# Kernel tuning notes

Measured on AMD Instinct MI355X. Metric: run time of the kernel, lower is better.

## Reference

```python
import jax, jax.numpy as jnp
import numpy as np

THRESHOLD = 1.0
CURRENT_DECAY = 0.5
VOLTAGE_DECAY = 0.5
WEIGHT_SCALE = 2.0  # slayer block weight_scale=2, weight_norm=False


def spike_fn(v):
    # Heaviside spike with hard threshold (forward only)
    return (v >= THRESHOLD).astype(v.dtype)


def conv_transpose_2d(x, w):
    # x: [NT, Cin, H, W]; w: [Cin, Cout, k, k] (pytorch ConvTranspose2d layout)
    # Equivalent dilated conv: swap in/out, flip spatial taps.
    rhs = jnp.transpose(w, (1, 0, 2, 3))[:, :, ::-1, ::-1]
    return jax.lax.conv_general_dilated(
        x, rhs, window_strides=(1, 1), padding=[(1, 1), (1, 1)],
        lhs_dilation=(2, 2), dimension_numbers=('NCHW', 'OIHW', 'NCHW'))


def cuba_block(x, w):
    # x: [N, Cin, H, W, T] -> spikes [N, Cout, 2H-1, 2W-1, T]
    N, Cin, H, W, T = x.shape
    xt = jnp.transpose(x, (4, 0, 1, 2, 3)).reshape(T * N, Cin, H, W)
    z = conv_transpose_2d(xt, WEIGHT_SCALE * w)  # synapse over all timesteps at once
    Cout, Ho, Wo = z.shape[1], z.shape[2], z.shape[3]
    z = z.reshape(T, N, Cout, Ho, Wo)

    def step(carry, zt):
        cur, vol = carry
        cur = (1.0 - CURRENT_DECAY) * cur + zt          # CUBA current dynamics
        vol = (1.0 - VOLTAGE_DECAY) * vol + cur          # CUBA voltage dynamics
        s = spike_fn(vol)
        vol = vol * (1.0 - s)                            # reset voltage on spike
        return (cur, vol), s

    init = (jnp.zeros_like(z[0]), jnp.zeros_like(z[0]))
    _, spikes = jax.lax.scan(step, init, z)              # [T, N, Cout, Ho, Wo]
    return jnp.transpose(spikes, (1, 2, 3, 4, 0))


def setup_inputs() -> dict:
    key = jax.random.key(0)
    k1, k2, k3, k4 = jax.random.split(key, 4)
    c_hid, C = 32, 2
    spike = (jax.random.uniform(k1, (4, c_hid * 4, 16, 16, 32)) < 0.3).astype(jnp.float32)

    def winit(k, cin, cout):
        return jax.random.normal(k, (cin, cout, 3, 3), jnp.float32) / np.sqrt(cin * 9.0)

    return {
        'spike': spike,
        'w1': winit(k2, c_hid * 4, c_hid * 2),
        'w2': winit(k3, c_hid * 2, c_hid),
        'w3': winit(k4, c_hid, C),
    }


def reference(spike, w1, w2, w3):
    counts = []
    for w in (w1, w2, w3):
        spike = cuba_block(spike, w)
        counts.append(jnp.mean(spike))
    return spike, jnp.stack(counts).reshape(1, -1)
```

## Files before the change

kernel.cpp:

```cpp
#include <hip/hip_runtime.h>

#define TT 32

__device__ __forceinline__ float bf16_bits_to_f32(unsigned short u) {
    unsigned v = ((unsigned)u) << 16; float f; __builtin_memcpy(&f, &v, 4); return f;
}
__device__ __forceinline__ unsigned short f32_to_bf16_rne(float f) {
    unsigned u; __builtin_memcpy(&u, &f, 4);
    u += 0x7FFFu + ((u >> 16) & 1u);
    return (unsigned short)(u >> 16);
}
__device__ __forceinline__ float round_bf16_f32(float f) {
    return bf16_bits_to_f32(f32_to_bf16_rne(f));
}
__device__ __forceinline__ float f64_to_bf16_f32(double d) {
    float fz = __double2float_rz(d);
    if ((double)fz != d) {
        unsigned u; __builtin_memcpy(&u, &fz, 4); u |= 1u; __builtin_memcpy(&fz, &u, 4);
    }
    return round_bf16_f32(fz);
}
__device__ __forceinline__ unsigned spread4(unsigned b) {
    unsigned x = (b | (b << 12)) & 0x000F000Fu;
    x = (x | (x << 6)) & 0x03030303u;
    x = (x | (x << 3)) & 0x11111111u;
    return x;
}

__global__ void detect_and_init(const unsigned* __restrict__ spk,
                                int* __restrict__ flag, float* __restrict__ sums)
{
    unsigned w = spk[threadIdx.x];
    bool ok = (w == 0u) || (w == 0x3F800000u);
    unsigned long long vote = __ballot(ok);
    if (threadIdx.x == 0) {
        flag[0] = (vote == 0xFFFFFFFFFFFFFFFFull) ? 0 : 1;
        sums[0] = 0.f; sums[1] = 0.f; sums[2] = 0.f;
    }
}

__global__ __launch_bounds__(256)
void pack_interleave(const void* __restrict__ ginv, unsigned* __restrict__ idx0,
                     const int* __restrict__ flag)
{
    const int gid = blockIdx.x * 256 + threadIdx.x;
    if (gid >= 32768) return;
    const int site = gid & 255;
    const int g    = (gid >> 8) & 31;
    const int n    = gid >> 13;

    unsigned m[4];
    #pragma unroll
    for (int k = 0; k < 4; ++k) {
        const size_t ebase = ((size_t)(n * 128 + 4 * g + k) * 256 + site) * TT;
        unsigned mask = 0u;
        if (flag[0]) {
            const uint4* p = (const uint4*)((const unsigned short*)ginv + ebase);
            #pragma unroll
            for (int q = 0; q < 4; ++q) {
                uint4 a = p[q];
                unsigned wd[4] = {a.x, a.y, a.z, a.w};
                #pragma unroll
                for (int mm = 0; mm < 4; ++mm) {
                    const int t = q * 8 + mm * 2;
                    mask |= (wd[mm] & 0xFFFFu) ? (1u << t)       : 0u;
                    mask |= (wd[mm] >> 16)     ? (1u << (t + 1)) : 0u;
                }
            }
        } else {
            const float4* p = (const float4*)((const float*)ginv + ebase);
            #pragma unroll
            for (int j = 0; j < 8; ++j) {
                float4 v = p[j];
                mask |= (v.x != 0.f) ? (1u << (j * 4 + 0)) : 0u;
                mask |= (v.y != 0.f) ? (1u << (j * 4 + 1)) : 0u;
                mask |= (v.z != 0.f) ? (1u << (j * 4 + 2)) : 0u;
                mask |= (v.w != 0.f) ? (1u << (j * 4 + 3)) : 0u;
            }
        }
        m[k] = mask;
    }
    unsigned w[4];
    #pragma unroll
    for (int q = 0; q < 4; ++q)
        w[q] =  spread4((m[0] >> (8 * q)) & 0xFFu)
             | (spread4((m[1] >> (8 * q)) & 0xFFu) << 1)
             | (spread4((m[2] >> (8 * q)) & 0xFFu) << 2)
             | (spread4((m[3] >> (8 * q)) & 0xFFu) << 3);
    *(uint2*)(idx0 + (size_t)gid * 2)           = make_uint2(w[0], w[1]);
    *(uint2*)(idx0 + (size_t)(32768 + gid) * 2) = make_uint2(w[2], w[3]);
}

template<int C, int PLANE>
__global__ __launch_bounds__(256)
void pack_mid_pairs(const unsigned* __restrict__ masks, unsigned* __restrict__ idx)
{
    constexpr int G = C / 4;
    constexpr int TOT = 4 * G * PLANE;
    const int gid = blockIdx.x * 256 + threadIdx.x;
    if (gid >= TOT) return;
    const int site = gid % PLANE;
    const int g    = (gid / PLANE) % G;
    const int n    = gid / (PLANE * G);
    unsigned m[4];
    #pragma unroll
    for (int k = 0; k < 4; ++k)
        m[k] = masks[(n * C + 4 * g + k) * PLANE + site];
    unsigned w[4];
    #pragma unroll
    for (int q = 0; q < 4; ++q)
        w[q] =  spread4((m[0] >> (8 * q)) & 0xFFu)
             | (spread4((m[1] >> (8 * q)) & 0xFFu) << 1)
             | (spread4((m[2] >> (8 * q)) & 0xFFu) << 2)
             | (spread4((m[3] >> (8 * q)) & 0xFFu) << 3);
    *(uint2*)(idx + (size_t)gid * 2)         = make_uint2(w[0], w[1]);
    *(uint2*)(idx + (size_t)(TOT + gid) * 2) = make_uint2(w[2], w[3]);
}

template<int C, int PLANE>
__global__ __launch_bounds__(256)
void pack_mid(const unsigned* __restrict__ masks, unsigned* __restrict__ idx)
{
    constexpr int G = C / 4;
    constexpr int TOT = 4 * G * PLANE;
    const int gid = blockIdx.x * 256 + threadIdx.x;
    if (gid >= TOT) return;
    const int site = gid % PLANE;
    const int g    = (gid / PLANE) % G;
    const int n    = gid / (PLANE * G);
    unsigned m[4];
    #pragma unroll
    for (int k = 0; k < 4; ++k)
        m[k] = masks[(n * C + 4 * g + k) * PLANE + site];
    #pragma unroll
    for (int q = 0; q < 4; ++q) {
        const unsigned w =  spread4((m[0] >> (8 * q)) & 0xFFu)
                         | (spread4((m[1] >> (8 * q)) & 0xFFu) << 1)
                         | (spread4((m[2] >> (8 * q)) & 0xFFu) << 2)
                         | (spread4((m[3] >> (8 * q)) & 0xFFu) << 3);
        idx[q * TOT + gid] = w;
    }
}

template<int CIN, int COUT>
__global__ __launch_bounds__(256)
void cuba_layer2(const unsigned* __restrict__ idxIn, const void* __restrict__ wptr,
                 unsigned* __restrict__ maskOut, int N, int Hi, int Wi,
                 float* __restrict__ sumOut, const int* __restrict__ flag)
{
    constexpr int G = CIN / 4;
    const bool isbf = (flag[0] != 0);
    const int Ho = 2 * Hi - 1, Wo = 2 * Wi - 1;
    const int co = (int)blockIdx.y;
    const int zz = 3 - (int)blockIdx.z;
    const int po = zz >> 1, pw = zz & 1;
    const int lg = po + pw;
    const int nTap = 1 << lg;
    const int nH = Hi - po, nW = Wi - pw;
    const int sites = N * nH * nW;
    const int siteBase = (int)blockIdx.x * 256;
    if (siteBase >= sites) return;

    __shared__ double lut[G][4][16];
    {
        const unsigned short* w16 = (const unsigned short*)wptr;
        const float* w32 = (const float*)wptr;
        const int entries = G * nTap * 16;
        for (int e = threadIdx.x; e < entries; e += 256) {
            const int idx = e & 15;
            const int tp  = (e >> 4) & (nTap - 1);
            const int g   = e >> (4 + lg);
            const int v = (po && (tp >= (pw ? 2 : 1))) ? 1 : 0;
            const int h = pw ? (tp & 1) : 0;
            const int kh = v ? 0 : (po ? 2 : 1);
            const int kw = h ? 0 : (pw ? 2 : 1);
            const int wof = kh * 3 + kw;
            double s = 0.0;
            #pragma unroll
            for (int k = 0; k < 4; ++k) {
                if ((idx >> k) & 1) {
                    const int wi = ((4 * g + k) * COUT + co) * 9 + wof;
                    const float wraw = isbf ? bf16_bits_to_f32(w16[wi]) : w32[wi];
                    s += 2.0 * (double)wraw;
                }
            }
            lut[g][tp][idx] = s;
        }
    }
    __syncthreads();

    const int siteIdx = siteBase + (int)threadIdx.x;
    float cnt = 0.f;

    if (siteIdx < sites) {
        const int b  = siteIdx % nW;
        const int t1 = siteIdx / nW;
        const int a  = t1 % nH;
        const int n  = t1 / nH;
        const int oh = 2 * a + po, ow = 2 * b + pw;
        const int plane = Hi * Wi;
        const int QT = N * G * plane;

        const int siteA = a * Wi + b;
        const int siteB = siteA + 1;
        const int siteC = siteA + Wi;
        const int siteD = siteC + 1;

        unsigned mask = 0u;
        float  curF = 0.f, volF = 0.f;
        double curD = 0.0, volD = 0.0;

        #pragma unroll 1
        for (int p = 0; p < 2; ++p) {
            double acc[16];
            #pragma unroll
            for (int j = 0; j < 16; ++j) acc[j] = 0.0;

            const unsigned* pb = idxIn + (size_t)(p * QT + n * G * plane) * 2;
            for (int g = 0; g < G; ++g) {
                const unsigned* bp = pb + (size_t)g * plane * 2;

                auto doTap = [&](int site, int tp) {
                    const uint2 wv = *(const uint2*)(bp + (size_t)site * 2);
                    const double* lp = &lut[g][tp][0];
                    #pragma unroll
                    for (int j = 0; j < 8; ++j)
                        acc[j] += lp[(wv.x >> (4 * j)) & 0xFu];
                    #pragma unroll
                    for (int j = 0; j < 8; ++j)
                        acc[8 + j] += lp[(wv.y >> (4 * j)) & 0xFu];
                };

                doTap(siteA, 0);
                if (pw) doTap(siteB, 1);
                if (po) {
                    doTap(siteC, pw ? 2 : 1);
                    if (pw) doTap(siteD, 3);
                }
            }

            if (isbf) {
                #pragma unroll
                for (int j = 0; j < 16; ++j) {
                    const int t = p * 16 + j;
                    const float z = f64_to_bf16_f32(acc[j]);
                    curF = round_bf16_f32(0.5f * curF + z);
                    volF = round_bf16_f32(0.5f * volF + curF);
                    const bool fire = (volF >= 1.0f);
                    mask |= fire ? (1u << t) : 0u;
                    volF = fire ? 0.f : volF;
                }
            } else {
                #pragma unroll
                for (int j = 0; j < 16; ++j) {
                    const int t = p * 16 + j;
                    curD = fma(0.5, curD, acc[j]);
                    volD = fma(0.5, volD, curD);
                    const bool fire = (volD >= 1.0);
                    mask |= fire ? (1u << t) : 0u;
                    volD = fire ? 0.0 : volD;
                }
            }
        }
        cnt = (float)__popc(mask);
        maskOut[((n * COUT + co) * Ho + oh) * Wo + ow] = mask;
    }

    #pragma unroll
    for (int o = 32; o >= 1; o >>= 1) cnt += __shfl_down(cnt, o);
    if ((threadIdx.x & 63) == 0 && cnt > 0.f) atomicAdd(sumOut, cnt);
}

template<int CIN, int COUT>
__global__ __launch_bounds__(256)
void cuba_layer_slab(const unsigned* __restrict__ idxIn, const void* __restrict__ wptr,
                     void* __restrict__ goutv, int N, int Hi, int Wi,
                     float* __restrict__ sumOut, const int* __restrict__ flag)
{
    constexpr int G = CIN / 4;
    const bool isbf = (flag[0] != 0);
    const int Ho = 2 * Hi - 1, Wo = 2 * Wi - 1;
    const int co = (int)blockIdx.y;
    const int zz = 3 - (int)blockIdx.z;
    const int po = zz >> 1, pw = zz & 1;
    const int lg = po + pw;
    const int nTap = 1 << lg;
    const int nH = Hi - po, nW = Wi - pw;
    const int sites = N * nH * nW;
    const int lS = lg;
    const int S  = 1 << lS;
    const int spb = 256 >> lS;
    const int siteBase = (int)blockIdx.x * spb;
    if (siteBase >= sites) return;

    __shared__ double lut[G][4][16];
    __shared__ double xch[1536];
    {
        const unsigned short* w16 = (const unsigned short*)wptr;
        const float* w32 = (const float*)wptr;
        const int entries = G * nTap * 16;
        for (int e = threadIdx.x; e < entries; e += 256) {
            const int idx = e & 15;
            const int tp  = (e >> 4) & (nTap - 1);
            const int g   = e >> (4 + lg);
            const int v = (po && (tp >= (pw ? 2 : 1))) ? 1 : 0;
            const int h = pw ? (tp & 1) : 0;
            const int kh = v ? 0 : (po ? 2 : 1);
            const int kw = h ? 0 : (pw ? 2 : 1);
            const int wof = kh * 3 + kw;
            double s = 0.0;
            #pragma unroll
            for (int k = 0; k < 4; ++k) {
                if ((idx >> k) & 1) {
                    const int wi = ((4 * g + k) * COUT + co) * 9 + wof;
                    const float wraw = isbf ? bf16_bits_to_f32(w16[wi]) : w32[wi];
                    s += 2.0 * (double)wraw;
                }
            }
            lut[g][tp][idx] = s;
        }
    }
    __syncthreads();

    const int slab = (int)threadIdx.x >> (8 - lS);
    const int sl   = (int)threadIdx.x & (spb - 1);
    const int siteIdx = siteBase + sl;
    const bool valid = siteIdx < sites;
    const int sIdx = valid ? siteIdx : 0;

    const int b  = sIdx % nW;
    const int t1v = sIdx / nW;
    const int a  = t1v % nH;
    const int n  = t1v / nH;
    const int oh = 2 * a + po, ow = 2 * b + pw;
    const int plane = Hi * Wi;
    const int QT = N * G * plane;

    const int siteA = a * Wi + b;
    const int siteB = siteA + 1;
    const int siteC = siteA + Wi;
    const int siteD = siteC + 1;

    int s1 = siteA, tp1 = 0;
    if (zz == 1)      { if (slab == 1) { s1 = siteB; tp1 = 1; } }
    else if (zz == 2) { if (slab == 1) { s1 = siteC; tp1 = 1; } }
    else if (zz == 3) {
        if      (slab == 1) { s1 = siteB; tp1 = 1; }
        else if (slab == 2) { s1 = siteC; tp1 = 2; }
        else if (slab == 3) { s1 = siteD; tp1 = 3; }
    }

    unsigned mask = 0u;
    float  curF = 0.f, volF = 0.f;
    double curD = 0.0, volD = 0.0;
    float cnt = 0.f;

    #pragma unroll 1
    for (int p = 0; p < 4; ++p) {
        double acc[8];
        #pragma unroll
        for (int j = 0; j < 8; ++j) acc[j] = 0.0;

        const unsigned* pb = idxIn + (size_t)p * QT + (size_t)(n * G) * plane;
        for (int g = 0; g < G; ++g) {
            const unsigned w1 = pb[(size_t)g * plane + s1];
            #pragma unroll
            for (int j = 0; j < 8; ++j)
                acc[j] += lut[g][tp1][(w1 >> (4 * j)) & 0xFu];
        }

        if (S > 1) {
            if (slab != 0) {
                #pragma unroll
                for (int j = 0; j < 8; ++j)
                    xch[(slab - 1) * (8 * spb) + j * spb + sl] = acc[j];
            }
            __syncthreads();
            if (slab == 0) {
                for (int s = 1; s < S; ++s)
                    #pragma unroll
                    for (int j = 0; j < 8; ++j)
                        acc[j] += xch[(s - 1) * (8 * spb) + j * spb + sl];
            }
        }

        if (slab == 0) {
            if (isbf) {
                #pragma unroll
                for (int j = 0; j < 8; ++j) {
                    const int t = p * 8 + j;
                    const float z = f64_to_bf16_f32(acc[j]);
                    curF = round_bf16_f32(0.5f * curF + z);
                    volF = round_bf16_f32(0.5f * volF + curF);
                    const bool fire = (volF >= 1.0f);
                    mask |= fire ? (1u << t) : 0u;
                    volF = fire ? 0.f : volF;
                }
            } else {
                #pragma unroll
                for (int j = 0; j < 8; ++j) {
                    const int t = p * 8 + j;
                    curD = fma(0.5, curD, acc[j]);
                    volD = fma(0.5, volD, curD);
                    const bool fire = (volD >= 1.0);
                    mask |= fire ? (1u << t) : 0u;
                    volD = fire ? 0.0 : volD;
                }
            }
        }
        if (S > 1) __syncthreads();
    }

    if (slab == 0 && valid) {
        cnt = (float)__popc(mask);
        const int gidOut = ((n * COUT + co) * Ho + oh) * Wo + ow;
        if (isbf) {
            uint4* ob = (uint4*)((unsigned short*)goutv + (size_t)gidOut * TT);
            #pragma unroll
            for (int q = 0; q < 4; ++q) {
                unsigned wd[4];
                #pragma unroll
                for (int m2 = 0; m2 < 4; ++m2) {
                    const int t = (q * 4 + m2) * 2;
                    wd[m2] = (((mask >> t) & 1u) ? 0x3F80u : 0u)
                           | (((mask >> (t + 1)) & 1u) ? 0x3F800000u : 0u);
                }
                ob[q] = make_uint4(wd[0], wd[1], wd[2], wd[3]);
            }
        } else {
            float4* ob = (float4*)((float*)goutv + (size_t)gidOut * TT);
            #pragma unroll
            for (int j = 0; j < 8; ++j) {
                float4 s4;
                s4.x = (mask >> (j * 4 + 0)) & 1u ? 1.0f : 0.0f;
                s4.y = (mask >> (j * 4 + 1)) & 1u ? 1.0f : 0.0f;
                s4.z = (mask >> (j * 4 + 2)) & 1u ? 1.0f : 0.0f;
                s4.w = (mask >> (j * 4 + 3)) & 1u ? 1.0f : 0.0f;
                ob[j] = s4;
            }
        }
    }

    #pragma unroll
    for (int o = 32; o >= 1; o >>= 1) cnt += __shfl_down(cnt, o);
    if ((threadIdx.x & 63) == 0 && cnt > 0.f) atomicAdd(sumOut, cnt);
}

__global__ void finalize_counts(const float* __restrict__ sums,
                                void* __restrict__ out, const int* __restrict__ flag)
{
    int i = threadIdx.x;
    if (i < 3) {
        const float numel[3] = {7872512.f, 15239168.f, 3748096.f};
        float v = sums[i] / numel[i];
        if (flag[0]) ((unsigned short*)out)[3748096 + i] = f32_to_bf16_rne(v);
        else         ((float*)out)[3748096 + i] = v;
    }
}

extern "C" void kernel_launch(void* const* d_in, const int* in_sizes, int n_in,
                              void* d_out, int out_size, void* d_ws, size_t ws_size,
                              hipStream_t stream)
{
    const void* x  = d_in[0];
    const void* w1 = d_in[1];
    const void* w2 = d_in[2];
    const void* w3 = d_in[3];

    unsigned* bufA = (unsigned*)d_ws;
    unsigned* bufB = bufA + 476288;
    unsigned* idx0 = bufB;
    float* sums = (float*)(bufB + 476288);
    int*   flag = (int*)(sums + 3);

    detect_and_init<<<1, 64, 0, stream>>>((const unsigned*)x, flag, sums);
    pack_interleave<<<128, 256, 0, stream>>>(x, idx0, flag);

    cuba_layer2<128, 64><<<dim3(4, 64, 4), 256, 0, stream>>>(
        idx0, w1, bufA, 4, 16, 16, sums + 0, flag);
    pack_mid_pairs<64, 961><<<241, 256, 0, stream>>>(bufA, bufB);
    cuba_layer2<64, 32><<<dim3(16, 32, 4), 256, 0, stream>>>(
        bufB, w2, bufA, 4, 31, 31, sums + 1, flag);
    pack_mid<32, 3721><<<466, 256, 0, stream>>>(bufA, bufB);
    cuba_layer_slab<32, 2><<<dim3(225, 2, 4), 256, 0, stream>>>(
        bufB, w3, d_out, 4, 61, 61, sums + 2, flag);

    finalize_counts<<<1, 64, 0, stream>>>(sums, d_out, flag);
}
```

Measured before the change: 419.7 us.

## Mix output parity classes across wavefronts in a block to balance tap work

The two transposed-conv layer kernels used to give each block a single output parity class, so blocks handling 4-tap sites ran far longer than 1-tap blocks. Now each of the four wavefronts in a block handles a different parity class, rotated by block index, with 64 sites per wavefront. The shared LUT is built for all 9 taps. The goal is to even out work per block and reduce the long tail of slow blocks. In exchange, wavefronts inside a block diverge in runtime, LUT setup work per block grows, and many more blocks each redo it.

```diff
diff --git a/kernel.cpp b/kernel.cpp
--- a/kernel.cpp
+++ b/kernel.cpp
@@ -144,37 +144,24 @@
 
 template<int CIN, int COUT>
 __global__ __launch_bounds__(256)
-void cuba_layer2(const unsigned* __restrict__ idxIn, const void* __restrict__ wptr,
-                 unsigned* __restrict__ maskOut, int N, int Hi, int Wi,
-                 float* __restrict__ sumOut, const int* __restrict__ flag)
+void cuba_layer_bal(const unsigned* __restrict__ idxIn, const void* __restrict__ wptr,
+                    unsigned* __restrict__ maskOut, int N, int Hi, int Wi,
+                    float* __restrict__ sumOut, const int* __restrict__ flag)
 {
     constexpr int G = CIN / 4;
     const bool isbf = (flag[0] != 0);
     const int Ho = 2 * Hi - 1, Wo = 2 * Wi - 1;
     const int co = (int)blockIdx.y;
-    const int zz = 3 - (int)blockIdx.z;
-    const int po = zz >> 1, pw = zz & 1;
-    const int lg = po + pw;
-    const int nTap = 1 << lg;
-    const int nH = Hi - po, nW = Wi - pw;
-    const int sites = N * nH * nW;
-    const int siteBase = (int)blockIdx.x * 256;
-    if (siteBase >= sites) return;
-
-    __shared__ double lut[G][4][16];
+
+    __shared__ double lut[G][9][16];
     {
         const unsigned short* w16 = (const unsigned short*)wptr;
         const float* w32 = (const float*)wptr;
-        const int entries = G * nTap * 16;
+        const int entries = G * 9 * 16;
         for (int e = threadIdx.x; e < entries; e += 256) {
             const int idx = e & 15;
-            const int tp  = (e >> 4) & (nTap - 1);
-            const int g   = e >> (4 + lg);
-            const int v = (po && (tp >= (pw ? 2 : 1))) ? 1 : 0;
-            const int h = pw ? (tp & 1) : 0;
-            const int kh = v ? 0 : (po ? 2 : 1);
-            const int kw = h ? 0 : (pw ? 2 : 1);
-            const int wof = kh * 3 + kw;
+            const int wof = (e >> 4) % 9;
+            const int g   = (e >> 4) / 9;
             double s = 0.0;
             #pragma unroll
             for (int k = 0; k < 4; ++k) {
@@ -184,12 +171,18 @@
                     s += 2.0 * (double)wraw;
                 }
             }
-            lut[g][tp][idx] = s;
+            lut[g][wof][idx] = s;
         }
     }
     __syncthreads();
 
-    const int siteIdx = siteBase + (int)threadIdx.x;
+    const int wv   = (int)threadIdx.x >> 6;
+    const int lane = (int)threadIdx.x & 63;
+    const int zz = (wv + (int)blockIdx.x + (int)blockIdx.y) & 3;
+    const int po = zz >> 1, pw = zz & 1;
+    const int nH = Hi - po, nW = Wi - pw;
+    const int sites = N * nH * nW;
+    const int siteIdx = (int)blockIdx.x * 64 + lane;
     float cnt = 0.f;
 
     if (siteIdx < sites) {
@@ -205,6 +198,10 @@
         const int siteB = siteA + 1;
         const int siteC = siteA + Wi;
         const int siteD = siteC + 1;
+        const int khA = po ? 2 : 1, kwA = pw ? 2 : 1;
+        const int wofA = khA * 3 + kwA;
+        const int wofB = khA * 3;
+        const int wofC = kwA;
 
         unsigned mask = 0u;
         float  curF = 0.f, volF = 0.f;
@@ -220,22 +217,22 @@
             for (int g = 0; g < G; ++g) {
                 const unsigned* bp = pb + (size_t)g * plane * 2;
 
-                auto doTap = [&](int site, int tp) {
-                    const uint2 wv = *(const uint2*)(bp + (size_t)site * 2);
-                    const double* lp = &lut[g][tp][0];
+                auto doTap = [&](int site, int wof) {
+                    const uint2 wvv = *(const uint2*)(bp + (size_t)site * 2);
+                    const double* lp = &lut[g][wof][0];
                     #pragma unroll
                     for (int j = 0; j < 8; ++j)
-                        acc[j] += lp[(wv.x >> (4 * j)) & 0xFu];
+                        acc[j] += lp[(wvv.x >> (4 * j)) & 0xFu];
                     #pragma unroll
                     for (int j = 0; j < 8; ++j)
-                        acc[8 + j] += lp[(wv.y >> (4 * j)) & 0xFu];
+                        acc[8 + j] += lp[(wvv.y >> (4 * j)) & 0xFu];
                 };
 
-                doTap(siteA, 0);
-                if (pw) doTap(siteB, 1);
+                doTap(siteA, wofA);
+                if (pw) doTap(siteB, wofB);
                 if (po) {
-                    doTap(siteC, pw ? 2 : 1);
-                    if (pw) doTap(siteD, 3);
+                    doTap(siteC, wofC);
+                    if (pw) doTap(siteD, 0);
                 }
             }
 
@@ -476,10 +473,10 @@
     detect_and_init<<<1, 64, 0, stream>>>((const unsigned*)x, flag, sums);
     pack_interleave<<<128, 256, 0, stream>>>(x, idx0, flag);
 
-    cuba_layer2<128, 64><<<dim3(4, 64, 4), 256, 0, stream>>>(
+    cuba_layer_bal<128, 64><<<dim3(16, 64), 256, 0, stream>>>(
         idx0, w1, bufA, 4, 16, 16, sums + 0, flag);
     pack_mid_pairs<64, 961><<<241, 256, 0, stream>>>(bufA, bufB);
-    cuba_layer2<64, 32><<<dim3(16, 32, 4), 256, 0, stream>>>(
+    cuba_layer_bal<64, 32><<<dim3(61, 32), 256, 0, stream>>>(
         bufB, w2, bufA, 4, 31, 31, sums + 1, flag);
     pack_mid<32, 3721><<<466, 256, 0, stream>>>(bufA, bufB);
     cuba_layer_slab<32, 2><<<dim3(225, 2, 4), 256, 0, stream>>>(
```

After: 411.5 us. About the same (-1.9%).
